# Kernel tuning notes

Measured on AMD Instinct MI355X. Metric: run time of the kernel, lower is better.

## Reference

```python
import jax, jax.numpy as jnp
import numpy as np

NEG_INF = -1e30  # stands in for -inf on the diagonal of the H-attention scores


def conv1x1(x, W, b):
    # x: [B,C,H,W], W: [O,C], b: [O] -> [B,O,H,W]
    return jnp.einsum('bchw,oc->bohw', x, W) + b[None, :, None, None]


def setup_inputs() -> dict:
    key = jax.random.key(0)
    ks = jax.random.split(key, 8)
    B, C, H, W = 8, 256, 128, 128
    Cqk = C // 8
    s = 0.02
    return {
        'x': jax.random.normal(ks[0], (B, C, H, W), jnp.float32),
        'Wq': jax.random.normal(ks[1], (Cqk, C), jnp.float32) * s,
        'bq': jnp.zeros((Cqk,), jnp.float32),
        'Wk': jax.random.normal(ks[2], (Cqk, C), jnp.float32) * s,
        'bk': jnp.zeros((Cqk,), jnp.float32),
        'Wv': jax.random.normal(ks[3], (C, C), jnp.float32) * s,
        'bv': jnp.zeros((C,), jnp.float32),
        'gamma': jax.random.normal(ks[4], (1,), jnp.float32),
    }


def reference(x, Wq, bq, Wk, bk, Wv, bv, gamma):
    B, C, H, W = x.shape
    q = conv1x1(x, Wq, bq)  # [B,Cqk,H,W]
    k = conv1x1(x, Wk, bk)  # [B,Cqk,H,W]
    v = conv1x1(x, Wv, bv)  # [B,C,H,W]

    # vertical (column) scores: energy_H[b,i,w,j] = <q[b,:,i,w], k[b,:,j,w]>
    eH = jnp.einsum('bciw,bcjw->biwj', q, k)
    diag = jnp.eye(H, dtype=bool)[:, None, :]  # [H,1,H] broadcast over w
    eH = jnp.where(diag[None], NEG_INF, eH)

    # horizontal (row) scores: energy_W[b,h,i,j] = <q[b,:,h,i], k[b,:,h,j]>
    eW = jnp.einsum('bchi,bchj->bhij', q, k)

    # joint softmax over the H+W criss-cross neighborhood
    att = jax.nn.softmax(jnp.concatenate([eH, eW], axis=3), axis=3)
    attH = att[..., :H]   # [b,i,w,j]
    attW = att[..., H:]   # [b,h,i,j]

    outH = jnp.einsum('bcjw,biwj->bciw', v, attH)
    outW = jnp.einsum('bchj,bhij->bchi', v, attW)
    return gamma[0] * (outH + outW) + x
```

## Files before the change

kernel.cpp:

```cpp
#include <hip/hip_runtime.h>
#include <hip/hip_bf16.h>

typedef __hip_bfloat16 bf16;
typedef __attribute__((ext_vector_type(8))) short bf16x8;
typedef __attribute__((ext_vector_type(4))) float f32x4;
typedef __attribute__((ext_vector_type(2))) float f32x2;
typedef unsigned int uint32;

#define NB 8
#define NC 256
#define NQK 32
#define NH 128
#define NW 128
#define NHW 16384
#define QSTR 40

static __device__ __forceinline__ float b2f(bf16 v){ return __bfloat162float(v); }
static __device__ __forceinline__ bf16  f2b(float v){ return __float2bfloat16(v); }
static __device__ __forceinline__ int swz(int row, int col){ return row*128 + (col ^ ((row&7)<<3)); }

static __device__ __forceinline__ uint32 pk_fp8x4(float a, float b, float c, float d){
    int v = __builtin_amdgcn_cvt_pk_fp8_f32(a, b, 0, false);
    v = __builtin_amdgcn_cvt_pk_fp8_f32(c, d, v, true);
    return (uint32)v;
}
static __device__ __forceinline__ bf16x8 up_fp8x8(uint2 u){
    f32x2 a = __builtin_amdgcn_cvt_pk_f32_fp8((int)u.x, false);
    f32x2 b = __builtin_amdgcn_cvt_pk_f32_fp8((int)u.x, true);
    f32x2 c = __builtin_amdgcn_cvt_pk_f32_fp8((int)u.y, false);
    f32x2 d = __builtin_amdgcn_cvt_pk_f32_fp8((int)u.y, true);
    union { bf16x8 v; bf16 h[8]; } r;
    r.h[0]=f2b(a[0]); r.h[1]=f2b(a[1]); r.h[2]=f2b(b[0]); r.h[3]=f2b(b[1]);
    r.h[4]=f2b(c[0]); r.h[5]=f2b(c[1]); r.h[6]=f2b(d[0]); r.h[7]=f2b(d[1]);
    return r.v;
}

__global__ __launch_bounds__(256) void k_prep(const float* __restrict__ Wq,
                                              const float* __restrict__ Wk,
                                              const float* __restrict__ Wv,
                                              bf16* __restrict__ wvb,
                                              bf16* __restrict__ wqkb){
    int idx = blockIdx.x*256 + threadIdx.x;
    if (idx < 65536){
        wvb[idx] = f2b(Wv[idx]);
    } else {
        int i2 = idx - 65536;
        wqkb[i2] = f2b(i2 < 8192 ? Wq[i2] : Wk[i2 - 8192]);
    }
}

__global__ __launch_bounds__(256) void k_tr(const float* __restrict__ x,
                                            unsigned char* __restrict__ xcm8,
                                            bf16* __restrict__ xbf){
    __shared__ float tile[64][65];
    int img = blockIdx.y;
    int tw = blockIdx.x & 1, th = blockIdx.x >> 1;
    int h0 = th*64, w0 = tw*64;
    int t = threadIdx.x;
    const float* src = x + (size_t)img*NHW;
    #pragma unroll
    for (int it=0; it<4; it++){
        int fl = it*256 + t;
        int row = fl >> 4, c4 = (fl & 15) * 4;
        float4 v = *(const float4*)(src + (size_t)(h0+row)*NW + w0 + c4);
        tile[row][c4+0]=v.x; tile[row][c4+1]=v.y; tile[row][c4+2]=v.z; tile[row][c4+3]=v.w;
    }
    __syncthreads();
    bf16* db = xbf + (size_t)img*NHW;
    #pragma unroll
    for (int it=0; it<4; it++){
        int fl = it*256 + t;
        int row = fl >> 4, c4 = (fl & 15) * 4;
        union { ushort4 u; bf16 h[4]; } pk;
        #pragma unroll
        for (int k2=0;k2<4;k2++) pk.h[k2] = f2b(tile[row][c4+k2]);
        *(ushort4*)(db + (size_t)(h0+row)*NW + w0 + c4) = pk.u;
    }
    unsigned char* dc = xcm8 + (size_t)img*NHW;
    #pragma unroll
    for (int it=0; it<4; it++){
        int fl = it*256 + t;
        int wl = fl >> 4, hq = (fl & 15) * 4;
        uint32 u = pk_fp8x4(tile[hq+0][wl], tile[hq+1][wl], tile[hq+2][wl], tile[hq+3][wl]);
        *(uint32*)(dc + (size_t)(w0+wl)*NH + h0 + hq) = u;
    }
}

__global__ __launch_bounds__(512) void k_qk(const bf16* __restrict__ xbf,
                                            const bf16* __restrict__ wqkb,
                                            const float* __restrict__ bq,
                                            const float* __restrict__ bk,
                                            bf16* __restrict__ qrw,
                                            bf16* __restrict__ krw){
    __shared__ __align__(16) bf16 Xl[256*QSTR];
    int t = threadIdx.x;
    int wv = t >> 6, l = t & 63, lr = l & 15, lg = l >> 4;
    int b = blockIdx.y;
    int p0 = blockIdx.x * 256;
    int q4 = t & 3, pb = ((t >> 2) & 63) * 4, chi = t >> 8;
    f32x4 acc[4][2] = {};
    for (int kb = 0; kb < 8; kb++){
        if (kb) __syncthreads();
        #pragma unroll
        for (int it = 0; it < 4; it++){
            int cl = it*8 + chi*4;
            const bf16* xp = xbf + ((size_t)(b*NC + kb*32 + cl + q4))*NHW + p0 + pb;
            union { ushort4 u; bf16 h[4]; } ld;
            ld.u = *(const ushort4*)xp;
            float e[4] = {b2f(ld.h[0]), b2f(ld.h[1]), b2f(ld.h[2]), b2f(ld.h[3])};
            float s1[4], s2[4];
            #pragma unroll
            for (int j=0;j<4;j++){
                float ex = __shfl_xor(e[j^1], 1);
                s1[j] = ((j&1)==(q4&1)) ? e[j] : ex;
            }
            #pragma unroll
            for (int j=0;j<4;j++){
                float ex = __shfl_xor(s1[j^2], 2);
                s2[j] = ((j&2)==(q4&2)) ? s1[j] : ex;
            }
            union { ushort4 u; bf16 h[4]; } pk;
            #pragma unroll
            for (int j=0;j<4;j++) pk.h[j] = f2b(s2[j]);
            *(ushort4*)(Xl + (pb + q4)*QSTR + cl) = pk.u;
        }
        __syncthreads();
        bf16x8 bf_[2];
        #pragma unroll
        for (int nt=0;nt<2;nt++)
            bf_[nt] = *(const bf16x8*)(Xl + (wv*32 + nt*16 + lr)*QSTR + lg*8);
        #pragma unroll
        for (int mt=0;mt<4;mt++){
            bf16x8 af = *(const bf16x8*)(wqkb + (size_t)(mt*16 + lr)*NC + kb*32 + lg*8);
            acc[mt][0] = __builtin_amdgcn_mfma_f32_16x16x32_bf16(af, bf_[0], acc[mt][0], 0,0,0);
            acc[mt][1] = __builtin_amdgcn_mfma_f32_16x16x32_bf16(af, bf_[1], acc[mt][1], 0,0,0);
        }
    }
    #pragma unroll
    for (int mt=0;mt<4;mt++){
        int o0 = mt*16 + lg*4;
        float4 bb = (mt < 2) ? *(const float4*)(bq + o0)
                             : *(const float4*)(bk + o0 - 32);
        bf16* dst = (mt < 2) ? qrw : krw;
        int oo = (mt < 2) ? o0 : o0 - 32;
        #pragma unroll
        for (int nt=0;nt<2;nt++){
            int p = p0 + wv*32 + nt*16 + lr;
            union { ushort4 u; bf16 h[4]; } pk;
            pk.h[0] = f2b(acc[mt][nt][0] + bb.x);
            pk.h[1] = f2b(acc[mt][nt][1] + bb.y);
            pk.h[2] = f2b(acc[mt][nt][2] + bb.z);
            pk.h[3] = f2b(acc[mt][nt][3] + bb.w);
            *(ushort4*)(dst + ((size_t)b*NHW + p)*NQK + oo) = pk.u;
        }
    }
}

__global__ __launch_bounds__(512) void k_colagg(const bf16* __restrict__ qrw,
                                                const bf16* __restrict__ krw,
                                                const unsigned char* __restrict__ xcm8,
                                                unsigned char* __restrict__ agg8,
                                                float* __restrict__ lH){
    __shared__ __align__(16) bf16 Pl[16384];
    __shared__ __align__(16) bf16 Xl[16384];
    __shared__ float lpart[1024];
    unsigned char* Xl8 = (unsigned char*)Xl;
    int t = threadIdx.x;
    int wv = t >> 6, l = t & 63, lr = l & 15, lg = l >> 4;
    int w = blockIdx.x, b = blockIdx.y;
    f32x4 zero = {0.f,0.f,0.f,0.f};
    bf16x8 kf = *(const bf16x8*)(krw + ((size_t)(b*NH + wv*16 + lr)*NW + w)*NQK + lg*8);
    float psum[8];
    int j0 = wv*16 + lg*4;
    for (int ni=0; ni<8; ni++){
        bf16x8 qf = *(const bf16x8*)(qrw + ((size_t)(b*NH + ni*16 + lr)*NW + w)*NQK + lg*8);
        f32x4 e = __builtin_amdgcn_mfma_f32_16x16x32_bf16(kf, qf, zero, 0,0,0);
        int i = ni*16 + lr;
        union { ushort4 u; bf16 h[4]; } pk;
        float ps = 0.f;
        #pragma unroll
        for (int r=0;r<4;r++){
            float pv = (j0 + r == i) ? 0.f : __expf(e[r]);
            pk.h[r] = f2b(pv);
            ps += pv;
        }
        *(ushort4*)&Pl[i*128 + (j0 ^ ((i&7)<<3))] = pk.u;
        ps += __shfl_xor(ps, 16);
        ps += __shfl_xor(ps, 32);
        psum[ni] = ps;
    }
    uint2 xg[4];
    #pragma unroll
    for (int it=0;it<4;it++){
        int fl = it*512 + t, c = fl >> 4, seg = fl & 15;
        xg[it] = *(const uint2*)(xcm8 + ((size_t)(b*NC + c)*NW + w)*NH + seg*8);
    }
    if (l < 16){
        #pragma unroll
        for (int ni=0;ni<8;ni++) lpart[wv*128 + ni*16 + lr] = psum[ni];
    }
    __syncthreads();
    if (t < 128){
        float s = 0.f;
        #pragma unroll
        for (int v=0;v<8;v++) s += lpart[v*128 + t];
        lH[((size_t)(b*NH + t))*NW + w] = s;
    }
    for (int half=0; half<2; half++){
        #pragma unroll
        for (int it=0;it<4;it++){
            int fl = it*512 + t, c = fl >> 4, seg = fl & 15;
            *(bf16x8*)&Xl[c*128 + ((seg*8) ^ ((c&7)<<3))] = up_fp8x8(xg[it]);
        }
        __syncthreads();
        if (half == 0){
            #pragma unroll
            for (int it=0;it<4;it++){
                int fl = it*512 + t, c = fl >> 4, seg = fl & 15;
                xg[it] = *(const uint2*)(xcm8 + ((size_t)(b*NC + 128 + c)*NW + w)*NH + seg*8);
            }
        }
        bf16x8 xa[4];
        #pragma unroll
        for (int kb=0;kb<4;kb++)
            xa[kb] = *(const bf16x8*)&Xl[swz(wv*16 + lr, kb*32 + lg*8)];
        f32x4 acc8[8];
        __builtin_amdgcn_s_setprio(1);
        for (int nj=0;nj<8;nj++){
            acc8[nj] = zero;
            #pragma unroll
            for (int kb=0;kb<4;kb++){
                bf16x8 pb = *(const bf16x8*)&Pl[swz(nj*16 + lr, kb*32 + lg*8)];
                acc8[nj] = __builtin_amdgcn_mfma_f32_16x16x32_bf16(xa[kb], pb, acc8[nj], 0,0,0);
            }
        }
        __builtin_amdgcn_s_setprio(0);
        __syncthreads();
        #pragma unroll
        for (int nj=0;nj<8;nj++){
            int i = nj*16 + lr, c4 = wv*16 + lg*4;
            *(uint32*)&Xl8[i*128 + (c4 ^ ((i&7)<<4))] =
                pk_fp8x4(acc8[nj][0], acc8[nj][1], acc8[nj][2], acc8[nj][3]);
        }
        __syncthreads();
        #pragma unroll
        for (int it=0;it<2;it++){
            int fl = it*512 + t, i = fl >> 3, seg = fl & 7;
            uint4 v = *(const uint4*)&Xl8[i*128 + ((seg*16) ^ ((i&7)<<4))];
            *(uint4*)(agg8 + ((size_t)(b*NHW + i*NW + w))*NC + half*128 + seg*16) = v;
        }
        if (half == 0) __syncthreads();
    }
}

__global__ __launch_bounds__(512) void k_rowfin(const bf16* __restrict__ qrw,
                                                const bf16* __restrict__ krw,
                                                const bf16* __restrict__ xbf,
                                                const unsigned char* __restrict__ agg8,
                                                const float* __restrict__ lH,
                                                const bf16* __restrict__ wvb,
                                                const float* __restrict__ bv,
                                                const float* __restrict__ gamma,
                                                float* __restrict__ out){
    __shared__ __align__(16) bf16 Pl[16384];
    __shared__ __align__(16) bf16 AggL[16384];
    __shared__ float lpart[1024];
    __shared__ __align__(16) float linv[128];
    int t = threadIdx.x;
    int wv = t >> 6, l = t & 63, lr = l & 15, lg = l >> 4;
    int h = blockIdx.x, b = blockIdx.y;
    f32x4 zero = {0.f,0.f,0.f,0.f};
    const size_t prow = (size_t)(b*NH + h)*NW;
    float lhv = (t < 128) ? lH[prow + t] : 0.f;
    bf16x8 kf = *(const bf16x8*)(krw + (prow + wv*16 + lr)*NQK + lg*8);
    float psum[8];
    int j0 = wv*16 + lg*4;
    for (int ni=0; ni<8; ni++){
        bf16x8 qf = *(const bf16x8*)(qrw + (prow + ni*16 + lr)*NQK + lg*8);
        f32x4 e = __builtin_amdgcn_mfma_f32_16x16x32_bf16(kf, qf, zero, 0,0,0);
        int i = ni*16 + lr;
        union { ushort4 u; bf16 h[4]; } pk;
        float ps = 0.f;
        #pragma unroll
        for (int r=0;r<4;r++){
            float pv = __expf(e[r]);
            pk.h[r] = f2b(pv);
            ps += pv;
        }
        *(ushort4*)&Pl[i*128 + (j0 ^ ((i&7)<<3))] = pk.u;
        ps += __shfl_xor(ps, 16);
        ps += __shfl_xor(ps, 32);
        psum[ni] = ps;
    }
    uint2 ag[4];
    #pragma unroll
    for (int it=0;it<4;it++){
        int fl = it*512 + t, i = fl >> 4, seg = fl & 15;
        ag[it] = *(const uint2*)(agg8 + (prow + i)*NC + seg*8);
    }
    bf16x8 xa[4];
    {
        const bf16* xr0 = xbf + ((size_t)(b*NC + wv*16 + lr))*NHW + h*NW;
        #pragma unroll
        for (int kb=0;kb<4;kb++) xa[kb] = *(const bf16x8*)(xr0 + kb*32 + lg*8);
    }
    if (l < 16){
        #pragma unroll
        for (int ni=0;ni<8;ni++) lpart[wv*128 + ni*16 + lr] = psum[ni];
    }
    __syncthreads();
    if (t < 128){
        float s = 0.f;
        #pragma unroll
        for (int v=0;v<8;v++) s += lpart[v*128 + t];
        linv[t] = 1.f/(lhv + s);
    }
    #pragma unroll
    for (int it=0;it<4;it++){
        int fl = it*512 + t, i = fl >> 4, seg = fl & 15;
        *(bf16x8*)&AggL[i*128 + ((seg*8) ^ ((i&7)<<3))] = up_fp8x8(ag[it]);
    }
    __syncthreads();
    f32x4 Facc[8][2] = {};
    for (int half=0; half<2; half++){
        if (half == 0){
            #pragma unroll
            for (int it=0;it<4;it++){
                int fl = it*512 + t, i = fl >> 4, seg = fl & 15;
                ag[it] = *(const uint2*)(agg8 + (prow + i)*NC + 128 + seg*8);
            }
        }
        __builtin_amdgcn_s_setprio(1);
        for (int nj=0;nj<8;nj++){
            f32x4 acc = zero;
            #pragma unroll
            for (int kb=0;kb<4;kb++){
                bf16x8 pb = *(const bf16x8*)&Pl[swz(nj*16 + lr, kb*32 + lg*8)];
                acc = __builtin_amdgcn_mfma_f32_16x16x32_bf16(xa[kb], pb, acc, 0,0,0);
            }
            int i = nj*16 + lr, c4 = wv*16 + lg*4;
            bf16* ap = &AggL[i*128 + (c4 ^ ((i&7)<<3))];
            union { ushort4 u; bf16 hh[4]; } old, nu;
            old.u = *(const ushort4*)ap;
            #pragma unroll
            for (int r=0;r<4;r++) nu.hh[r] = f2b(b2f(old.hh[r]) + acc[r]);
            *(ushort4*)ap = nu.u;
        }
        __builtin_amdgcn_s_setprio(0);
        __syncthreads();
        bf16x8 xb2[4];
        if (half == 0){
            const bf16* xr1 = xbf + ((size_t)(b*NC + 128 + wv*16 + lr))*NHW + h*NW;
            #pragma unroll
            for (int kb=0;kb<4;kb++) xb2[kb] = *(const bf16x8*)(xr1 + kb*32 + lg*8);
        }
        __builtin_amdgcn_s_setprio(1);
        for (int kb2=0; kb2<4; kb2++){
            bf16x8 bw[2];
            #pragma unroll
            for (int nt=0;nt<2;nt++)
                bw[nt] = *(const bf16x8*)(wvb + (size_t)(wv*32 + nt*16 + lr)*NC + half*128 + kb2*32 + lg*8);
            #pragma unroll
            for (int pt=0;pt<8;pt++){
                bf16x8 aa = *(const bf16x8*)&AggL[swz(pt*16 + lr, kb2*32 + lg*8)];
                Facc[pt][0] = __builtin_amdgcn_mfma_f32_16x16x32_bf16(aa, bw[0], Facc[pt][0], 0,0,0);
                Facc[pt][1] = __builtin_amdgcn_mfma_f32_16x16x32_bf16(aa, bw[1], Facc[pt][1], 0,0,0);
            }
        }
        __builtin_amdgcn_s_setprio(0);
        if (half == 0){
            __syncthreads();
            #pragma unroll
            for (int it=0;it<4;it++){
                int fl = it*512 + t, i = fl >> 4, seg = fl & 15;
                *(bf16x8*)&AggL[i*128 + ((seg*8) ^ ((i&7)<<3))] = up_fp8x8(ag[it]);
            }
            #pragma unroll
            for (int kb=0;kb<4;kb++) xa[kb] = xb2[kb];
            __syncthreads();
        }
    }
    float g = gamma[0];
    #pragma unroll
    for (int nt=0;nt<2;nt++){
        int co = wv*32 + nt*16 + lr;
        float gb = g*bv[co];
        const bf16* xr   = xbf + ((size_t)(b*NC + co))*NHW + h*NW;
        float*      orow = out + ((size_t)(b*NC + co))*NHW + h*NW;
        #pragma unroll
        for (int pt=0;pt<8;pt++){
            int p4 = pt*16 + lg*4;
            float4 lv = *(const float4*)&linv[p4];
            union { ushort4 u; bf16 hh[4]; } xv;
            xv.u = *(const ushort4*)(xr + p4);
            float4 ov;
            ov.x = g*lv.x*Facc[pt][nt][0] + gb + b2f(xv.hh[0]);
            ov.y = g*lv.y*Facc[pt][nt][1] + gb + b2f(xv.hh[1]);
            ov.z = g*lv.z*Facc[pt][nt][2] + gb + b2f(xv.hh[2]);
            ov.w = g*lv.w*Facc[pt][nt][3] + gb + b2f(xv.hh[3]);
            *(float4*)(orow + p4) = ov;
        }
    }
}

extern "C" void kernel_launch(void* const* d_in, const int* in_sizes, int n_in,
                              void* d_out, int out_size, void* d_ws, size_t ws_size,
                              hipStream_t stream){
    (void)in_sizes; (void)n_in; (void)out_size; (void)ws_size;
    const float* x     = (const float*)d_in[0];
    const float* Wq    = (const float*)d_in[1];
    const float* bq    = (const float*)d_in[2];
    const float* Wk    = (const float*)d_in[3];
    const float* bk    = (const float*)d_in[4];
    const float* Wv    = (const float*)d_in[5];
    const float* bv    = (const float*)d_in[6];
    const float* gamma = (const float*)d_in[7];
    float* out = (float*)d_out;
    char* ws = (char*)d_ws;

    bf16*          qrw  = (bf16*)          (ws + 0);
    bf16*          krw  = (bf16*)          (ws + 8388608);
    unsigned char* xcm8 = (unsigned char*) (ws + 16777216);
    bf16*          xbf  = (bf16*)          (ws + 50331648);
    float*         lH   = (float*)         (ws + 117440512);
    bf16*          wvb  = (bf16*)          (ws + 117964800);
    bf16*          wqkb = (bf16*)          (ws + 118095872);
    unsigned char* agg8 = (unsigned char*) (ws + 118128640);

    k_prep  <<<dim3(320),     dim3(256), 0, stream>>>(Wq, Wk, Wv, wvb, wqkb);
    k_tr    <<<dim3(4, 2048), dim3(256), 0, stream>>>(x, xcm8, xbf);
    k_qk    <<<dim3(64, 8),   dim3(512), 0, stream>>>(xbf, wqkb, bq, bk, qrw, krw);
    k_colagg<<<dim3(128, 8),  dim3(512), 0, stream>>>(qrw, krw, xcm8, agg8, lH);
    k_rowfin<<<dim3(128, 8),  dim3(512), 0, stream>>>(qrw, krw, xbf, agg8, lH, wvb, bv, gamma, out);
}
```

Baseline: 197.8 us.

## Switch attention score and aggregation MFMAs to FP8 with interleaved FP8 Q/K

Q and K are now stored as FP8 in one interleaved 64-byte-per-pixel buffer instead of two bf16 buffers. The score MFMAs and the P·X aggregation MFMAs in both the column and row kernels use fp8×fp8 instructions, with probabilities and X tiles kept in FP8 in shared memory under a 16-row swizzle. The goals are less global traffic for Q/K, half the LDS footprint for Pl/Xl (which, with launch_bounds(512,6), allows more resident blocks), and no FP8-to-bf16 upconversion of X. The cost is lower precision in the exponentiated scores and in the aggregation, which adds accuracy risk.

```diff
diff --git a/kernel.cpp b/kernel.cpp
--- a/kernel.cpp
+++ b/kernel.cpp
@@ -6,10 +6,10 @@
 typedef __attribute__((ext_vector_type(4))) float f32x4;
 typedef __attribute__((ext_vector_type(2))) float f32x2;
 typedef unsigned int uint32;
+typedef long long i64;
 
 #define NB 8
 #define NC 256
-#define NQK 32
 #define NH 128
 #define NW 128
 #define NHW 16384
@@ -18,6 +18,7 @@
 static __device__ __forceinline__ float b2f(bf16 v){ return __bfloat162float(v); }
 static __device__ __forceinline__ bf16  f2b(float v){ return __float2bfloat16(v); }
 static __device__ __forceinline__ int swz(int row, int col){ return row*128 + (col ^ ((row&7)<<3)); }
+static __device__ __forceinline__ int swz8(int row, int col){ return row*128 + (col ^ ((row&15)<<3)); }
 
 static __device__ __forceinline__ uint32 pk_fp8x4(float a, float b, float c, float d){
     int v = __builtin_amdgcn_cvt_pk_fp8_f32(a, b, 0, false);
@@ -33,6 +34,16 @@
     r.h[0]=f2b(a[0]); r.h[1]=f2b(a[1]); r.h[2]=f2b(b[0]); r.h[3]=f2b(b[1]);
     r.h[4]=f2b(c[0]); r.h[5]=f2b(c[1]); r.h[6]=f2b(d[0]); r.h[7]=f2b(d[1]);
     return r.v;
+}
+static __device__ __forceinline__ i64 u2ll(uint2 u){
+    union { uint2 a; i64 b; } c; c.a = u; return c.b;
+}
+static __device__ __forceinline__ i64 bf8_to_fp8(bf16x8 v){
+    union { bf16x8 v8; bf16 h[8]; } a; a.v8 = v;
+    uint2 r;
+    r.x = pk_fp8x4(b2f(a.h[0]), b2f(a.h[1]), b2f(a.h[2]), b2f(a.h[3]));
+    r.y = pk_fp8x4(b2f(a.h[4]), b2f(a.h[5]), b2f(a.h[6]), b2f(a.h[7]));
+    return u2ll(r);
 }
 
 __global__ __launch_bounds__(256) void k_prep(const float* __restrict__ Wq,
@@ -90,8 +101,7 @@
                                             const bf16* __restrict__ wqkb,
                                             const float* __restrict__ bq,
                                             const float* __restrict__ bk,
-                                            bf16* __restrict__ qrw,
-                                            bf16* __restrict__ krw){
+                                            unsigned char* __restrict__ qk8){
     __shared__ __align__(16) bf16 Xl[256*QSTR];
     int t = threadIdx.x;
     int wv = t >> 6, l = t & 63, lr = l & 15, lg = l >> 4;
@@ -141,50 +151,42 @@
         int o0 = mt*16 + lg*4;
         float4 bb = (mt < 2) ? *(const float4*)(bq + o0)
                              : *(const float4*)(bk + o0 - 32);
-        bf16* dst = (mt < 2) ? qrw : krw;
-        int oo = (mt < 2) ? o0 : o0 - 32;
         #pragma unroll
         for (int nt=0;nt<2;nt++){
             int p = p0 + wv*32 + nt*16 + lr;
-            union { ushort4 u; bf16 h[4]; } pk;
-            pk.h[0] = f2b(acc[mt][nt][0] + bb.x);
-            pk.h[1] = f2b(acc[mt][nt][1] + bb.y);
-            pk.h[2] = f2b(acc[mt][nt][2] + bb.z);
-            pk.h[3] = f2b(acc[mt][nt][3] + bb.w);
-            *(ushort4*)(dst + ((size_t)b*NHW + p)*NQK + oo) = pk.u;
-        }
-    }
-}
-
-__global__ __launch_bounds__(512) void k_colagg(const bf16* __restrict__ qrw,
-                                                const bf16* __restrict__ krw,
-                                                const unsigned char* __restrict__ xcm8,
-                                                unsigned char* __restrict__ agg8,
-                                                float* __restrict__ lH){
-    __shared__ __align__(16) bf16 Pl[16384];
-    __shared__ __align__(16) bf16 Xl[16384];
+            uint32 v = pk_fp8x4(acc[mt][nt][0] + bb.x, acc[mt][nt][1] + bb.y,
+                                acc[mt][nt][2] + bb.z, acc[mt][nt][3] + bb.w);
+            *(uint32*)(qk8 + ((size_t)b*NHW + p)*64 + o0) = v;
+        }
+    }
+}
+
+__global__ __launch_bounds__(512, 6) void k_colagg(const unsigned char* __restrict__ qk8,
+                                                   const unsigned char* __restrict__ xcm8,
+                                                   unsigned char* __restrict__ agg8,
+                                                   float* __restrict__ lH){
+    __shared__ __align__(16) unsigned char Pl8[16384];
+    __shared__ __align__(16) unsigned char Xl8[16384];
     __shared__ float lpart[1024];
-    unsigned char* Xl8 = (unsigned char*)Xl;
     int t = threadIdx.x;
     int wv = t >> 6, l = t & 63, lr = l & 15, lg = l >> 4;
     int w = blockIdx.x, b = blockIdx.y;
     f32x4 zero = {0.f,0.f,0.f,0.f};
-    bf16x8 kf = *(const bf16x8*)(krw + ((size_t)(b*NH + wv*16 + lr)*NW + w)*NQK + lg*8);
+    const unsigned char* qkb = qk8 + (size_t)b*NHW*64;
+    i64 kf8 = u2ll(*(const uint2*)(qkb + ((size_t)((wv*16 + lr)*NW + w))*64 + 32 + lg*8));
     float psum[8];
     int j0 = wv*16 + lg*4;
     for (int ni=0; ni<8; ni++){
-        bf16x8 qf = *(const bf16x8*)(qrw + ((size_t)(b*NH + ni*16 + lr)*NW + w)*NQK + lg*8);
-        f32x4 e = __builtin_amdgcn_mfma_f32_16x16x32_bf16(kf, qf, zero, 0,0,0);
+        i64 qf8 = u2ll(*(const uint2*)(qkb + ((size_t)((ni*16 + lr)*NW + w))*64 + lg*8));
+        f32x4 e = __builtin_amdgcn_mfma_f32_16x16x32_fp8_fp8(kf8, qf8, zero, 0,0,0);
         int i = ni*16 + lr;
-        union { ushort4 u; bf16 h[4]; } pk;
-        float ps = 0.f;
+        float pv[4], ps = 0.f;
         #pragma unroll
         for (int r=0;r<4;r++){
-            float pv = (j0 + r == i) ? 0.f : __expf(e[r]);
-            pk.h[r] = f2b(pv);
-            ps += pv;
-        }
-        *(ushort4*)&Pl[i*128 + (j0 ^ ((i&7)<<3))] = pk.u;
+            pv[r] = (j0 + r == i) ? 0.f : __expf(e[r]);
+            ps += pv[r];
+        }
+        *(uint32*)&Pl8[i*128 + (j0 ^ ((i&15)<<3))] = pk_fp8x4(pv[0],pv[1],pv[2],pv[3]);
         ps += __shfl_xor(ps, 16);
         ps += __shfl_xor(ps, 32);
         psum[ni] = ps;
@@ -210,7 +212,7 @@
         #pragma unroll
         for (int it=0;it<4;it++){
             int fl = it*512 + t, c = fl >> 4, seg = fl & 15;
-            *(bf16x8*)&Xl[c*128 + ((seg*8) ^ ((c&7)<<3))] = up_fp8x8(xg[it]);
+            *(uint2*)&Xl8[c*128 + ((seg*8) ^ ((c&15)<<3))] = xg[it];
         }
         __syncthreads();
         if (half == 0){
@@ -220,18 +222,18 @@
                 xg[it] = *(const uint2*)(xcm8 + ((size_t)(b*NC + 128 + c)*NW + w)*NH + seg*8);
             }
         }
-        bf16x8 xa[4];
+        i64 xa8[4];
         #pragma unroll
         for (int kb=0;kb<4;kb++)
-            xa[kb] = *(const bf16x8*)&Xl[swz(wv*16 + lr, kb*32 + lg*8)];
+            xa8[kb] = u2ll(*(const uint2*)&Xl8[swz8(wv*16 + lr, kb*32 + lg*8)]);
         f32x4 acc8[8];
         __builtin_amdgcn_s_setprio(1);
         for (int nj=0;nj<8;nj++){
             acc8[nj] = zero;
             #pragma unroll
             for (int kb=0;kb<4;kb++){
-                bf16x8 pb = *(const bf16x8*)&Pl[swz(nj*16 + lr, kb*32 + lg*8)];
-                acc8[nj] = __builtin_amdgcn_mfma_f32_16x16x32_bf16(xa[kb], pb, acc8[nj], 0,0,0);
+                i64 pb8 = u2ll(*(const uint2*)&Pl8[swz8(nj*16 + lr, kb*32 + lg*8)]);
+                acc8[nj] = __builtin_amdgcn_mfma_f32_16x16x32_fp8_fp8(xa8[kb], pb8, acc8[nj], 0,0,0);
             }
         }
         __builtin_amdgcn_s_setprio(0);
@@ -239,55 +241,51 @@
         #pragma unroll
         for (int nj=0;nj<8;nj++){
             int i = nj*16 + lr, c4 = wv*16 + lg*4;
-            *(uint32*)&Xl8[i*128 + (c4 ^ ((i&7)<<4))] =
+            *(uint32*)&Xl8[i*128 + (c4 ^ ((i&15)<<3))] =
                 pk_fp8x4(acc8[nj][0], acc8[nj][1], acc8[nj][2], acc8[nj][3]);
         }
         __syncthreads();
         #pragma unroll
-        for (int it=0;it<2;it++){
-            int fl = it*512 + t, i = fl >> 3, seg = fl & 7;
-            uint4 v = *(const uint4*)&Xl8[i*128 + ((seg*16) ^ ((i&7)<<4))];
-            *(uint4*)(agg8 + ((size_t)(b*NHW + i*NW + w))*NC + half*128 + seg*16) = v;
+        for (int it=0;it<4;it++){
+            int fl = it*512 + t, i = fl >> 4, seg = fl & 15;
+            uint2 v = *(const uint2*)&Xl8[i*128 + ((seg*8) ^ ((i&15)<<3))];
+            *(uint2*)(agg8 + ((size_t)(b*NHW + i*NW + w))*NC + half*128 + seg*8) = v;
         }
         if (half == 0) __syncthreads();
     }
 }
 
-__global__ __launch_bounds__(512) void k_rowfin(const bf16* __restrict__ qrw,
-                                                const bf16* __restrict__ krw,
-                                                const bf16* __restrict__ xbf,
-                                                const unsigned char* __restrict__ agg8,
-                                                const float* __restrict__ lH,
-                                                const bf16* __restrict__ wvb,
-                                                const float* __restrict__ bv,
-                                                const float* __restrict__ gamma,
-                                                float* __restrict__ out){
-    __shared__ __align__(16) bf16 Pl[16384];
+__global__ __launch_bounds__(512, 6) void k_rowfin(const unsigned char* __restrict__ qk8,
+                                                   const bf16* __restrict__ xbf,
+                                                   const unsigned char* __restrict__ agg8,
+                                                   const float* __restrict__ lH,
+                                                   const bf16* __restrict__ wvb,
+                                                   const float* __restrict__ bv,
+                                                   const float* __restrict__ gamma,
+                                                   float* __restrict__ out){
+    __shared__ __align__(16) unsigned char Pl8[16384];
     __shared__ __align__(16) bf16 AggL[16384];
-    __shared__ float lpart[1024];
-    __shared__ __align__(16) float linv[128];
+    __shared__ __align__(16) float lpart[1024];
     int t = threadIdx.x;
     int wv = t >> 6, l = t & 63, lr = l & 15, lg = l >> 4;
     int h = blockIdx.x, b = blockIdx.y;
     f32x4 zero = {0.f,0.f,0.f,0.f};
     const size_t prow = (size_t)(b*NH + h)*NW;
     float lhv = (t < 128) ? lH[prow + t] : 0.f;
-    bf16x8 kf = *(const bf16x8*)(krw + (prow + wv*16 + lr)*NQK + lg*8);
+    i64 kf8 = u2ll(*(const uint2*)(qk8 + (prow + wv*16 + lr)*64 + 32 + lg*8));
     float psum[8];
     int j0 = wv*16 + lg*4;
     for (int ni=0; ni<8; ni++){
-        bf16x8 qf = *(const bf16x8*)(qrw + (prow + ni*16 + lr)*NQK + lg*8);
-        f32x4 e = __builtin_amdgcn_mfma_f32_16x16x32_bf16(kf, qf, zero, 0,0,0);
+        i64 qf8 = u2ll(*(const uint2*)(qk8 + (prow + ni*16 + lr)*64 + lg*8));
+        f32x4 e = __builtin_amdgcn_mfma_f32_16x16x32_fp8_fp8(kf8, qf8, zero, 0,0,0);
         int i = ni*16 + lr;
-        union { ushort4 u; bf16 h[4]; } pk;
-        float ps = 0.f;
+        float pv[4], ps = 0.f;
         #pragma unroll
         for (int r=0;r<4;r++){
-            float pv = __expf(e[r]);
-            pk.h[r] = f2b(pv);
-            ps += pv;
-        }
-        *(ushort4*)&Pl[i*128 + (j0 ^ ((i&7)<<3))] = pk.u;
+            pv[r] = __expf(e[r]);
+            ps += pv[r];
+        }
+        *(uint32*)&Pl8[i*128 + (j0 ^ ((i&15)<<3))] = pk_fp8x4(pv[0],pv[1],pv[2],pv[3]);
         ps += __shfl_xor(ps, 16);
         ps += __shfl_xor(ps, 32);
         psum[ni] = ps;
@@ -298,11 +296,11 @@
         int fl = it*512 + t, i = fl >> 4, seg = fl & 15;
         ag[it] = *(const uint2*)(agg8 + (prow + i)*NC + seg*8);
     }
-    bf16x8 xa[4];
+    i64 xa8[4];
     {
         const bf16* xr0 = xbf + ((size_t)(b*NC + wv*16 + lr))*NHW + h*NW;
         #pragma unroll
-        for (int kb=0;kb<4;kb++) xa[kb] = *(const bf16x8*)(xr0 + kb*32 + lg*8);
+        for (int kb=0;kb<4;kb++) xa8[kb] = bf8_to_fp8(*(const bf16x8*)(xr0 + kb*32 + lg*8));
     }
     if (l < 16){
         #pragma unroll
@@ -313,7 +311,7 @@
         float s = 0.f;
         #pragma unroll
         for (int v=0;v<8;v++) s += lpart[v*128 + t];
-        linv[t] = 1.f/(lhv + s);
+        lpart[t] = 1.f/(lhv + s);
     }
     #pragma unroll
     for (int it=0;it<4;it++){
@@ -335,8 +333,8 @@
             f32x4 acc = zero;
             #pragma unroll
             for (int kb=0;kb<4;kb++){
-                bf16x8 pb = *(const bf16x8*)&Pl[swz(nj*16 + lr, kb*32 + lg*8)];
-                acc = __builtin_amdgcn_mfma_f32_16x16x32_bf16(xa[kb], pb, acc, 0,0,0);
+                i64 pb8 = u2ll(*(const uint2*)&Pl8[swz8(nj*16 + lr, kb*32 + lg*8)]);
+                acc = __builtin_amdgcn_mfma_f32_16x16x32_fp8_fp8(xa8[kb], pb8, acc, 0,0,0);
             }
             int i = nj*16 + lr, c4 = wv*16 + lg*4;
             bf16* ap = &AggL[i*128 + (c4 ^ ((i&7)<<3))];
@@ -348,11 +346,11 @@
         }
         __builtin_amdgcn_s_setprio(0);
         __syncthreads();
-        bf16x8 xb2[4];
+        i64 xb2[4];
         if (half == 0){
             const bf16* xr1 = xbf + ((size_t)(b*NC + 128 + wv*16 + lr))*NHW + h*NW;
             #pragma unroll
-            for (int kb=0;kb<4;kb++) xb2[kb] = *(const bf16x8*)(xr1 + kb*32 + lg*8);
+            for (int kb=0;kb<4;kb++) xb2[kb] = bf8_to_fp8(*(const bf16x8*)(xr1 + kb*32 + lg*8));
         }
         __builtin_amdgcn_s_setprio(1);
         for (int kb2=0; kb2<4; kb2++){
@@ -376,7 +374,7 @@
                 *(bf16x8*)&AggL[i*128 + ((seg*8) ^ ((i&7)<<3))] = up_fp8x8(ag[it]);
             }
             #pragma unroll
-            for (int kb=0;kb<4;kb++) xa[kb] = xb2[kb];
+            for (int kb=0;kb<4;kb++) xa8[kb] = xb2[kb];
             __syncthreads();
         }
     }
@@ -390,7 +388,7 @@
         #pragma unroll
         for (int pt=0;pt<8;pt++){
             int p4 = pt*16 + lg*4;
-            float4 lv = *(const float4*)&linv[p4];
+            float4 lv = *(const float4*)&lpart[p4];
             union { ushort4 u; bf16 hh[4]; } xv;
             xv.u = *(const ushort4*)(xr + p4);
             float4 ov;
@@ -418,18 +416,17 @@
     float* out = (float*)d_out;
     char* ws = (char*)d_ws;
 
-    bf16*          qrw  = (bf16*)          (ws + 0);
-    bf16*          krw  = (bf16*)          (ws + 8388608);
-    unsigned char* xcm8 = (unsigned char*) (ws + 16777216);
-    bf16*          xbf  = (bf16*)          (ws + 50331648);
-    float*         lH   = (float*)         (ws + 117440512);
-    bf16*          wvb  = (bf16*)          (ws + 117964800);
-    bf16*          wqkb = (bf16*)          (ws + 118095872);
-    unsigned char* agg8 = (unsigned char*) (ws + 118128640);
+    unsigned char* qk8  = (unsigned char*) (ws + 0);
+    unsigned char* xcm8 = (unsigned char*) (ws + 8388608);
+    bf16*          xbf  = (bf16*)          (ws + 41943040);
+    float*         lH   = (float*)         (ws + 109051904);
+    bf16*          wvb  = (bf16*)          (ws + 109576192);
+    bf16*          wqkb = (bf16*)          (ws + 109707264);
+    unsigned char* agg8 = (unsigned char*) (ws + 109740032);
 
     k_prep  <<<dim3(320),     dim3(256), 0, stream>>>(Wq, Wk, Wv, wvb, wqkb);
     k_tr    <<<dim3(4, 2048), dim3(256), 0, stream>>>(x, xcm8, xbf);
-    k_qk    <<<dim3(64, 8),   dim3(512), 0, stream>>>(xbf, wqkb, bq, bk, qrw, krw);
-    k_colagg<<<dim3(128, 8),  dim3(512), 0, stream>>>(qrw, krw, xcm8, agg8, lH);
-    k_rowfin<<<dim3(128, 8),  dim3(512), 0, stream>>>(qrw, krw, xbf, agg8, lH, wvb, bv, gamma, out);
-}
+    k_qk    <<<dim3(64, 8),   dim3(512), 0, stream>>>(xbf, wqkb, bq, bk, qk8);
+    k_colagg<<<dim3(128, 8),  dim3(512), 0, stream>>>(qk8, xcm8, agg8, lH);
+    k_rowfin<<<dim3(128, 8),  dim3(512), 0, stream>>>(qk8, xbf, agg8, lH, wvb, bv, gamma, out);
+}
```

Result: slower. 444.4 us (+124.6%).
